# Kernel optimization log

Hardware: AMD Instinct MI355X
Metric: run time of the kernel (lower is better)

Reference implementation:

```python
import jax, jax.numpy as jnp
import numpy as np

EPS = 1e-5
NUM_HEADS = 8

def layer_norm(x, w, b):
    mu = jnp.mean(x, axis=-1, keepdims=True)
    var = jnp.mean(jnp.square(x - mu), axis=-1, keepdims=True)
    return (x - mu) * jax.lax.rsqrt(var + EPS) * w + b

def setup_inputs() -> dict:
    key = jax.random.key(0)
    B, N, C, H, W = 8, 8, 256, 64, 64
    ks = jax.random.split(key, 16)
    p = lambda k, shape: (jax.random.normal(k, shape, dtype=jnp.float32) * 0.02)
    return {
        "mask_tokens": jax.random.normal(ks[0], (B, N, C), dtype=jnp.float32),
        "prompt_embeddings": jax.random.normal(ks[1], (N, B, C, H, W), dtype=jnp.float32),
        "ln_t_w": jnp.ones((C,), jnp.float32), "ln_t_b": jnp.zeros((C,), jnp.float32),
        "ln_p_w": jnp.ones((C,), jnp.float32), "ln_p_b": jnp.zeros((C,), jnp.float32),
        "Wq": p(ks[2], (C, C)), "bq": jnp.zeros((C,), jnp.float32),
        "Wk": p(ks[3], (C, C)), "bk": jnp.zeros((C,), jnp.float32),
        "Wv": p(ks[4], (C, C)), "bv": jnp.zeros((C,), jnp.float32),
        "Wo": p(ks[5], (C, C)), "bo": jnp.zeros((C,), jnp.float32),
        "W1": p(ks[6], (2 * C, C)), "b1": jnp.zeros((2 * C,), jnp.float32),
        "W2": p(ks[7], (C, 2 * C)), "b2": jnp.zeros((C,), jnp.float32),
    }

def reference(mask_tokens, prompt_embeddings, ln_t_w, ln_t_b, ln_p_w, ln_p_b,
              Wq, bq, Wk, bk, Wv, bv, Wo, bo, W1, b1, W2, b2):
    B, N, C = mask_tokens.shape
    Hh = NUM_HEADS
    dh = C // Hh
    scale = 1.0 / jnp.sqrt(jnp.asarray(dh, mask_tokens.dtype))

    normed_tokens = layer_norm(mask_tokens, ln_t_w, ln_t_b)  # [B,N,C]

    # prompt_embeddings: [N,B,C,H,W] -> flatten spatial, move to [B,N,S,C]
    Np, Bp, Cp, H, W = prompt_embeddings.shape
    S = H * W
    prompts = prompt_embeddings.reshape(Np, Bp, Cp, S).transpose(1, 0, 3, 2)  # [B,N,S,C]
    normed_prompts = layer_norm(prompts, ln_p_w, ln_p_b)

    # single-query cross attention per (batch, mask-token), batched over N
    q = (normed_tokens @ Wq.T + bq).reshape(B, N, Hh, dh)          # [B,N,H,dh]
    k = (normed_prompts @ Wk.T + bk).reshape(B, N, S, Hh, dh)       # [B,N,S,H,dh]
    v = (normed_prompts @ Wv.T + bv).reshape(B, N, S, Hh, dh)

    scores = jnp.einsum('bnhd,bnshd->bnhs', q, k) * scale           # [B,N,H,S]
    attn = jax.nn.softmax(scores, axis=-1)
    ctx = jnp.einsum('bnhs,bnshd->bnhd', attn, v).reshape(B, N, C)  # [B,N,C]
    attended = ctx @ Wo.T + bo

    updated = mask_tokens + attended
    hidden = jax.nn.relu(updated @ W1.T + b1)                       # [B,N,2C]
    mlp_out = hidden @ W2.T + b2
    return updated + mlp_out
```

## Files before the change

kernel.cpp:

```cpp
#include <hip/hip_runtime.h>
#include <math.h>

#define C 256
#define S 4096
#define NH 8
#define NSG 64
#define EPS 1e-5f
#define SCALE 0.17677669529663687f

#define TSTR 72
#define PTSTR 72

#define OFF_GWP 0
#define OFF_G   65536
#define OFF_BC  66048
#define OFF_LP  66560
#define OFF_ZP  99328
#define OFF_WEI 132096
#define OFF_MP  263168

typedef __attribute__((ext_vector_type(8))) short short8;
typedef __attribute__((ext_vector_type(4))) float f32x4;
typedef __attribute__((ext_vector_type(4))) float nfloat4;

__device__ __forceinline__ float bf_lo(unsigned int u) {
    return __builtin_bit_cast(float, u << 16);
}
__device__ __forceinline__ float bf_hi(unsigned int u) {
    return __builtin_bit_cast(float, u & 0xffff0000u);
}
__device__ __forceinline__ unsigned int bf_pack(float a, float b) {
    unsigned int ua = (__builtin_bit_cast(unsigned int, a) + 0x8000u) >> 16;
    unsigned int ub = (__builtin_bit_cast(unsigned int, b) + 0x8000u) & 0xffff0000u;
    return ua | ub;
}
__device__ __forceinline__ float bf_round(float a) {
    unsigned int u = (__builtin_bit_cast(unsigned int, a) + 0x8000u) & 0xffff0000u;
    return __builtin_bit_cast(float, u);
}

__global__ __launch_bounds__(256) void k1_prep(
    const float* __restrict__ mt, const float* __restrict__ ln_t_w, const float* __restrict__ ln_t_b,
    const float* __restrict__ ln_p_w, const float* __restrict__ ln_p_b,
    const float* __restrict__ Wq, const float* __restrict__ bq,
    const float* __restrict__ Wk, const float* __restrict__ bk,
    unsigned int* __restrict__ gwp, float* __restrict__ Gv, float* __restrict__ Bc)
{
    int bn  = blockIdx.x;
    int tid = threadIdx.x;
    int wid = tid >> 6, lane = tid & 63;
    __shared__ float nt[C];
    __shared__ float qv[C];
    __shared__ float wks[NH][C];
    __shared__ float red[8];

    float x  = mt[bn * C + tid];
    float s1 = x, s2 = x * x;
    #pragma unroll
    for (int off = 32; off; off >>= 1) {
        s1 += __shfl_xor(s1, off);
        s2 += __shfl_xor(s2, off);
    }
    if (lane == 0) { red[wid] = s1; red[4 + wid] = s2; }
    __syncthreads();
    float mu   = (red[0] + red[1] + red[2] + red[3]) * (1.0f / C);
    float msq  = (red[4] + red[5] + red[6] + red[7]) * (1.0f / C);
    float rstd = rsqrtf(msq - mu * mu + EPS);
    nt[tid] = (x - mu) * rstd * ln_t_w[tid] + ln_t_b[tid];
    __syncthreads();

    {
        float acc = bq[tid];
        const float* wrow = Wq + (size_t)tid * C;
        #pragma unroll 8
        for (int c = 0; c < C; ++c) acc += nt[c] * wrow[c];
        qv[tid] = acc;
    }
    __syncthreads();

    int c = tid;
    #pragma unroll
    for (int h = 0; h < NH; ++h) {
        float a = 0.f;
        #pragma unroll 4
        for (int d = 0; d < 32; ++d) a += qv[h * 32 + d] * Wk[(size_t)(h * 32 + d) * C + c];
        wks[h][c] = a * SCALE;
    }
    __syncthreads();

    for (int i = tid; i < C * 4; i += 256) {
        int cc = i >> 2, pr = i & 3;
        float g0 = ln_p_w[cc] * wks[pr * 2][cc];
        float g1 = ln_p_w[cc] * wks[pr * 2 + 1][cc];
        gwp[(size_t)bn * C * 4 + i] = bf_pack(g0, g1);
    }

    {
        int h = tid >> 5, l32 = tid & 31;
        float g = 0.f, bs = 0.f;
        #pragma unroll
        for (int cc = l32; cc < C; cc += 32) {
            float w = wks[h][cc];
            g  += bf_round(ln_p_w[cc] * w);
            bs += ln_p_b[cc] * w;
        }
        float qb = qv[h * 32 + l32] * bk[h * 32 + l32];
        #pragma unroll
        for (int off = 16; off; off >>= 1) {
            g  += __shfl_xor(g, off);
            bs += __shfl_xor(bs, off);
            qb += __shfl_xor(qb, off);
        }
        if (l32 == 0) {
            Gv[bn * NH + h] = g;
            Bc[bn * NH + h] = bs + qb * SCALE;
        }
    }
}

__global__ __launch_bounds__(256, 3) void kfused(
    const float* __restrict__ pe, const unsigned int* __restrict__ gwp,
    const float* __restrict__ Gv, const float* __restrict__ Bc,
    float* __restrict__ LP, float* __restrict__ ZP, float* __restrict__ Mp)
{
    int blk = blockIdx.x;
    int swz = (blk & 7) * 512 + (blk >> 3);
    int bn  = swz >> 6;
    int sg  = swz & 63;
    int tid = threadIdx.x;
    int w = tid >> 6, lane = tid & 63;
    int cg = lane >> 4, l16 = lane & 15;
    int b = bn >> 3, n = bn & 7;
    const float* xb = pe + ((size_t)(n * 8 + b)) * C * S;
    int s0 = sg * 64;

    __shared__ unsigned short tile[C * TSTR];
    __shared__ unsigned short ptT[16 * PTSTR];
    __shared__ float pbuf[4][64][10];
    __shared__ uint4 gwt[C];

    {
        const uint4* src = reinterpret_cast<const uint4*>(gwp + (size_t)bn * C * 4);
        gwt[tid] = src[tid];
        for (int i = tid; i < 8 * PTSTR; i += 256) ptT[8 * PTSTR + i] = 0;
    }
    __syncthreads();

    {
        const float* xq = xb + (size_t)(w * 64 + cg) * S + s0 + l16 * 4;
        nfloat4 xr[16];
        #pragma unroll
        for (int j = 0; j < 16; ++j)
            xr[j] = __builtin_nontemporal_load(
                        reinterpret_cast<const nfloat4*>(xq + (size_t)(4 * j) * S));

        float sum[4] = {0.f,0.f,0.f,0.f}, sq[4] = {0.f,0.f,0.f,0.f};
        float A[4][NH];
        #pragma unroll
        for (int e = 0; e < 4; ++e)
            #pragma unroll
            for (int h = 0; h < NH; ++h) A[e][h] = 0.f;

        #pragma unroll
        for (int j = 0; j < 16; ++j) {
            int c = w * 64 + 4 * j + cg;
            uint2 pk;
            pk.x = bf_pack(xr[j].x, xr[j].y);
            pk.y = bf_pack(xr[j].z, xr[j].w);
            *reinterpret_cast<uint2*>(&tile[c * TSTR + l16 * 4]) = pk;
            uint4 g = gwt[c];
            float xe[4] = {xr[j].x, xr[j].y, xr[j].z, xr[j].w};
            #pragma unroll
            for (int e = 0; e < 4; ++e) {
                float xx = xe[e];
                sum[e] += xx;
                sq[e]  += xx * xx;
                A[e][0] += bf_lo(g.x) * xx; A[e][1] += bf_hi(g.x) * xx;
                A[e][2] += bf_lo(g.y) * xx; A[e][3] += bf_hi(g.y) * xx;
                A[e][4] += bf_lo(g.z) * xx; A[e][5] += bf_hi(g.z) * xx;
                A[e][6] += bf_lo(g.w) * xx; A[e][7] += bf_hi(g.w) * xx;
            }
        }
        #pragma unroll
        for (int e = 0; e < 4; ++e) {
            sum[e] += __shfl_xor(sum[e], 16); sum[e] += __shfl_xor(sum[e], 32);
            sq[e]  += __shfl_xor(sq[e],  16); sq[e]  += __shfl_xor(sq[e],  32);
            #pragma unroll
            for (int h = 0; h < NH; ++h) {
                A[e][h] += __shfl_xor(A[e][h], 16);
                A[e][h] += __shfl_xor(A[e][h], 32);
            }
        }
        if (cg == 0) {
            #pragma unroll
            for (int e = 0; e < 4; ++e) {
                float* pb = &pbuf[w][l16 * 4 + e][0];
                pb[0] = sum[e];
                pb[1] = sq[e];
                #pragma unroll
                for (int h = 0; h < NH; ++h) pb[2 + h] = A[e][h];
            }
        }
    }
    __syncthreads();

    if (tid < 64) {
        int s = tid;
        float sum = 0.f, sq = 0.f;
        float A[NH];
        #pragma unroll
        for (int h = 0; h < NH; ++h) A[h] = 0.f;
        #pragma unroll
        for (int wv = 0; wv < 4; ++wv) {
            const float* pb = &pbuf[wv][s][0];
            sum += pb[0];
            sq  += pb[1];
            #pragma unroll
            for (int h = 0; h < NH; ++h) A[h] += pb[2 + h];
        }
        float mu   = sum * (1.f / C);
        float var  = sq * (1.f / C) - mu * mu;
        float rs   = rsqrtf(var + EPS);
        float murv = mu * rs;

        float l8[NH], z8[NH];
        #pragma unroll
        for (int h = 0; h < NH; ++h) {
            float p = __expf(rs * A[h] - murv * Gv[bn * NH + h] + Bc[bn * NH + h]);
            ptT[h * PTSTR + s] = (unsigned short)(bf_pack(p * rs, 0.f) & 0xffffu);
            l8[h] = p;
            z8[h] = p * murv;
        }
        #pragma unroll
        for (int h = 0; h < NH; ++h) {
            float l = l8[h], zz = z8[h];
            #pragma unroll
            for (int off = 32; off; off >>= 1) {
                l  += __shfl_xor(l,  off);
                zz += __shfl_xor(zz, off);
            }
            if (tid == 0) {
                LP[(size_t)(bn * NH + h) * NSG + sg] = l;
                ZP[(size_t)(bn * NH + h) * NSG + sg] = zz;
            }
        }
    }
    __syncthreads();

    {
        int mrow = lane & 15;
        int kgrp = lane >> 4;
        float* mp = Mp + (((size_t)sg * 64 + bn) * C) * NH;
        #pragma unroll
        for (int ct = 0; ct < 4; ++ct) {
            int ctile = w * 4 + ct;
            int crow  = ctile * 16 + mrow;
            f32x4 acc = {0.f, 0.f, 0.f, 0.f};
            #pragma unroll
            for (int kc = 0; kc < 2; ++kc) {
                uint4 ap = *reinterpret_cast<const uint4*>(&tile[crow * TSTR + kc * 32 + kgrp * 8]);
                uint4 bp = *reinterpret_cast<const uint4*>(&ptT[mrow * PTSTR + kc * 32 + kgrp * 8]);
                short8 af  = __builtin_bit_cast(short8, ap);
                short8 bfv = __builtin_bit_cast(short8, bp);
                acc = __builtin_amdgcn_mfma_f32_16x16x32_bf16(af, bfv, acc, 0, 0, 0);
            }
            if (mrow < NH) {
                #pragma unroll
                for (int r = 0; r < 4; ++r) {
                    int cl = ctile * 16 + kgrp * 4 + r;
                    mp[cl * NH + mrow] = acc[r];
                }
            }
        }
    }
}

__global__ __launch_bounds__(256) void kfoldM(
    const float* __restrict__ Mp, const float* __restrict__ LP, const float* __restrict__ ZP,
    const float* __restrict__ lpw, const float* __restrict__ lpb, float* __restrict__ weig)
{
    int blk = blockIdx.x;
    int bn = blk >> 3, slice = blk & 7;
    int tid = threadIdx.x;
    __shared__ float ilz[2 * NH];

    if (tid < NH) {
        float L = 0.f, Z = 0.f;
        #pragma unroll 8
        for (int j = 0; j < NSG; ++j) {
            L += LP[(size_t)(bn * NH + tid) * NSG + j];
            Z += ZP[(size_t)(bn * NH + tid) * NSG + j];
        }
        float inv = 1.f / L;
        ilz[tid]      = inv;
        ilz[NH + tid] = Z * inv;
    }
    __syncthreads();

    int c0 = slice * 32;
    const float* base = Mp + ((size_t)bn * C + c0) * NH + tid;
    float acc = 0.f;
    #pragma unroll 8
    for (int sg = 0; sg < NSG; ++sg)
        acc += base[(size_t)sg * 64 * C * NH];

    int c = c0 + (tid >> 3), h = tid & 7;
    weig[(size_t)bn * NH * C + h * C + c] = lpw[c] * (acc * ilz[h] - ilz[NH + h]) + lpb[c];
}

__global__ __launch_bounds__(256) void kpost(
    const float* __restrict__ mt, const float* __restrict__ weig,
    const float* __restrict__ Wv, const float* __restrict__ bv,
    const float* __restrict__ Wo, const float* __restrict__ bo,
    const float* __restrict__ W1, const float* __restrict__ b1,
    const float* __restrict__ W2, const float* __restrict__ b2,
    float* __restrict__ out)
{
    int bn  = blockIdx.x;
    int tid = threadIdx.x;
    __shared__ float wei[NH * C];
    __shared__ float ctxs[C];
    __shared__ float upds[C];
    __shared__ float hid[2 * C];

    for (int v = tid; v < 512; v += 256)
        *reinterpret_cast<float4*>(&wei[v * 4]) =
            *reinterpret_cast<const float4*>(weig + (size_t)bn * NH * C + v * 4);
    __syncthreads();

    {
        int h = tid >> 5;
        float a = bv[tid];
        const float* wrow = Wv + (size_t)tid * C;
        const float* wh   = wei + h * C;
        #pragma unroll 16
        for (int c2 = 0; c2 < C; ++c2) a += wh[c2] * wrow[c2];
        ctxs[tid] = a;
    }
    __syncthreads();

    float att = bo[tid];
    {
        const float* wrow = Wo + (size_t)tid * C;
        #pragma unroll 16
        for (int j = 0; j < C; ++j) att += ctxs[j] * wrow[j];
    }
    float upd = mt[(size_t)bn * C + tid] + att;
    upds[tid] = upd;
    __syncthreads();

    #pragma unroll
    for (int r = 0; r < 2; ++r) {
        int k = tid + r * 256;
        float a = b1[k];
        const float* wrow = W1 + (size_t)k * C;
        #pragma unroll 16
        for (int c2 = 0; c2 < C; ++c2) a += upds[c2] * wrow[c2];
        hid[k] = fmaxf(a, 0.f);
    }
    __syncthreads();

    float a = b2[tid];
    const float* wrow = W2 + (size_t)tid * 2 * C;
    #pragma unroll 16
    for (int k = 0; k < 2 * C; ++k) a += hid[k] * wrow[k];
    out[(size_t)bn * C + tid] = upd + a;
}

extern "C" void kernel_launch(void* const* d_in, const int* in_sizes, int n_in,
                              void* d_out, int out_size, void* d_ws, size_t ws_size,
                              hipStream_t stream)
{
    const float* mt  = (const float*)d_in[0];
    const float* pe  = (const float*)d_in[1];
    const float* ltw = (const float*)d_in[2];
    const float* ltb = (const float*)d_in[3];
    const float* lpw = (const float*)d_in[4];
    const float* lpb = (const float*)d_in[5];
    const float* Wq  = (const float*)d_in[6];
    const float* bq  = (const float*)d_in[7];
    const float* Wk  = (const float*)d_in[8];
    const float* bk  = (const float*)d_in[9];
    const float* Wv  = (const float*)d_in[10];
    const float* bv  = (const float*)d_in[11];
    const float* Wo  = (const float*)d_in[12];
    const float* bo  = (const float*)d_in[13];
    const float* W1  = (const float*)d_in[14];
    const float* b1  = (const float*)d_in[15];
    const float* W2  = (const float*)d_in[16];
    const float* b2  = (const float*)d_in[17];

    float* ws   = (float*)d_ws;
    float* outp = (float*)d_out;

    unsigned int* gwp = (unsigned int*)(ws + OFF_GWP);
    float* Gv         = ws + OFF_G;
    float* Bc         = ws + OFF_BC;
    float* LP         = ws + OFF_LP;
    float* ZP         = ws + OFF_ZP;
    float* weig       = ws + OFF_WEI;
    float* Mp         = ws + OFF_MP;

    k1_prep<<<64,   256, 0, stream>>>(mt, ltw, ltb, lpw, lpb, Wq, bq, Wk, bk, gwp, Gv, Bc);
    kfused <<<4096, 256, 0, stream>>>(pe, gwp, Gv, Bc, LP, ZP, Mp);
    kfoldM <<<512,  256, 0, stream>>>(Mp, LP, ZP, lpw, lpb, weig);
    kpost  <<<64,   256, 0, stream>>>(mt, weig, Wv, bv, Wo, bo, W1, b1, W2, b2, outp);
}
```

Measured before the change: 147.8 us.

## Double spatial tile per block in fused attention kernel, halving grid and partials

Each kfused block now handles 128 spatial positions instead of 64, loading two column strips per thread with 32 float4 loads in flight. Grid shrinks to 2048 blocks, the MFMA K-loop doubles, and the Mp partial count that kfoldM must reduce halves. Softmax partials are still kept per 64-position strip. Launch bounds drop from 3 to 1 block per CU, and the tile LDS grows to about 68 KB. This risks lower occupancy and less latency hiding for the memory-bound stream, in exchange for more work per block and less partial traffic.

```diff
diff --git a/kernel.cpp b/kernel.cpp
--- a/kernel.cpp
+++ b/kernel.cpp
@@ -4,12 +4,13 @@
 #define C 256
 #define S 4096
 #define NH 8
-#define NSG 64
+#define NSGM 32
+#define NSTRIP 64
 #define EPS 1e-5f
 #define SCALE 0.17677669529663687f
 
-#define TSTR 72
-#define PTSTR 72
+#define TSTR 136
+#define PTSTR 136
 
 #define OFF_GWP 0
 #define OFF_G   65536
@@ -118,25 +119,25 @@
     }
 }
 
-__global__ __launch_bounds__(256, 3) void kfused(
+__global__ __launch_bounds__(256, 1) void kfused(
     const float* __restrict__ pe, const unsigned int* __restrict__ gwp,
     const float* __restrict__ Gv, const float* __restrict__ Bc,
     float* __restrict__ LP, float* __restrict__ ZP, float* __restrict__ Mp)
 {
     int blk = blockIdx.x;
-    int swz = (blk & 7) * 512 + (blk >> 3);
-    int bn  = swz >> 6;
-    int sg  = swz & 63;
+    int swz = (blk & 7) * 256 + (blk >> 3);
+    int bn  = swz >> 5;
+    int sg  = swz & 31;
     int tid = threadIdx.x;
     int w = tid >> 6, lane = tid & 63;
     int cg = lane >> 4, l16 = lane & 15;
     int b = bn >> 3, n = bn & 7;
     const float* xb = pe + ((size_t)(n * 8 + b)) * C * S;
-    int s0 = sg * 64;
+    int s0 = sg * 128;
 
     __shared__ unsigned short tile[C * TSTR];
     __shared__ unsigned short ptT[16 * PTSTR];
-    __shared__ float pbuf[4][64][10];
+    __shared__ float pbuf[4][128][11];
     __shared__ uint4 gwt[C];
 
     {
@@ -148,63 +149,95 @@
 
     {
         const float* xq = xb + (size_t)(w * 64 + cg) * S + s0 + l16 * 4;
-        nfloat4 xr[16];
-        #pragma unroll
-        for (int j = 0; j < 16; ++j)
-            xr[j] = __builtin_nontemporal_load(
-                        reinterpret_cast<const nfloat4*>(xq + (size_t)(4 * j) * S));
-
-        float sum[4] = {0.f,0.f,0.f,0.f}, sq[4] = {0.f,0.f,0.f,0.f};
-        float A[4][NH];
+        nfloat4 x0a[8], x1a[8], x0b[8], x1b[8];
+        #pragma unroll
+        for (int q = 0; q < 8; ++q) {
+            const float* p = xq + (size_t)(4 * q) * S;
+            x0a[q] = __builtin_nontemporal_load(reinterpret_cast<const nfloat4*>(p));
+            x1a[q] = __builtin_nontemporal_load(reinterpret_cast<const nfloat4*>(p + 64));
+        }
+        #pragma unroll
+        for (int q = 0; q < 8; ++q) {
+            const float* p = xq + (size_t)(4 * (q + 8)) * S;
+            x0b[q] = __builtin_nontemporal_load(reinterpret_cast<const nfloat4*>(p));
+            x1b[q] = __builtin_nontemporal_load(reinterpret_cast<const nfloat4*>(p + 64));
+        }
+
+        float sum0[4] = {0,0,0,0}, sq0[4] = {0,0,0,0};
+        float sum1[4] = {0,0,0,0}, sq1[4] = {0,0,0,0};
+        float A0[4][NH], A1[4][NH];
         #pragma unroll
         for (int e = 0; e < 4; ++e)
             #pragma unroll
-            for (int h = 0; h < NH; ++h) A[e][h] = 0.f;
-
-        #pragma unroll
-        for (int j = 0; j < 16; ++j) {
-            int c = w * 64 + 4 * j + cg;
-            uint2 pk;
-            pk.x = bf_pack(xr[j].x, xr[j].y);
-            pk.y = bf_pack(xr[j].z, xr[j].w);
-            *reinterpret_cast<uint2*>(&tile[c * TSTR + l16 * 4]) = pk;
-            uint4 g = gwt[c];
-            float xe[4] = {xr[j].x, xr[j].y, xr[j].z, xr[j].w};
+            for (int h = 0; h < NH; ++h) { A0[e][h] = 0.f; A1[e][h] = 0.f; }
+
+        #define PROC(X0, X1, QB)                                                     \
+        {                                                                            \
+            _Pragma("unroll")                                                        \
+            for (int q = 0; q < 8; ++q) {                                            \
+                int cc = w * 64 + 4 * (q + QB) + cg;                                 \
+                uint2 pk0, pk1;                                                      \
+                pk0.x = bf_pack(X0[q].x, X0[q].y);                                   \
+                pk0.y = bf_pack(X0[q].z, X0[q].w);                                   \
+                pk1.x = bf_pack(X1[q].x, X1[q].y);                                   \
+                pk1.y = bf_pack(X1[q].z, X1[q].w);                                   \
+                *reinterpret_cast<uint2*>(&tile[cc * TSTR + l16 * 4]) = pk0;         \
+                *reinterpret_cast<uint2*>(&tile[cc * TSTR + 64 + l16 * 4]) = pk1;    \
+                uint4 g = gwt[cc];                                                   \
+                float ge[8] = {bf_lo(g.x), bf_hi(g.x), bf_lo(g.y), bf_hi(g.y),       \
+                               bf_lo(g.z), bf_hi(g.z), bf_lo(g.w), bf_hi(g.w)};     \
+                float xe0[4] = {X0[q].x, X0[q].y, X0[q].z, X0[q].w};                 \
+                float xe1[4] = {X1[q].x, X1[q].y, X1[q].z, X1[q].w};                 \
+                _Pragma("unroll")                                                    \
+                for (int e = 0; e < 4; ++e) {                                        \
+                    float xx0 = xe0[e], xx1 = xe1[e];                                \
+                    sum0[e] += xx0; sq0[e] += xx0 * xx0;                             \
+                    sum1[e] += xx1; sq1[e] += xx1 * xx1;                             \
+                    _Pragma("unroll")                                                \
+                    for (int h = 0; h < NH; ++h) {                                   \
+                        A0[e][h] += ge[h] * xx0;                                     \
+                        A1[e][h] += ge[h] * xx1;                                     \
+                    }                                                                \
+                }                                                                    \
+            }                                                                        \
+        }
+        PROC(x0a, x1a, 0)
+        PROC(x0b, x1b, 8)
+        #undef PROC
+
+        #pragma unroll
+        for (int e = 0; e < 4; ++e) {
+            sum0[e] += __shfl_xor(sum0[e], 16); sum0[e] += __shfl_xor(sum0[e], 32);
+            sq0[e]  += __shfl_xor(sq0[e],  16); sq0[e]  += __shfl_xor(sq0[e],  32);
+            sum1[e] += __shfl_xor(sum1[e], 16); sum1[e] += __shfl_xor(sum1[e], 32);
+            sq1[e]  += __shfl_xor(sq1[e],  16); sq1[e]  += __shfl_xor(sq1[e],  32);
+            #pragma unroll
+            for (int h = 0; h < NH; ++h) {
+                A0[e][h] += __shfl_xor(A0[e][h], 16);
+                A0[e][h] += __shfl_xor(A0[e][h], 32);
+                A1[e][h] += __shfl_xor(A1[e][h], 16);
+                A1[e][h] += __shfl_xor(A1[e][h], 32);
+            }
+        }
+        if (cg == 0) {
             #pragma unroll
             for (int e = 0; e < 4; ++e) {
-                float xx = xe[e];
-                sum[e] += xx;
-                sq[e]  += xx * xx;
-                A[e][0] += bf_lo(g.x) * xx; A[e][1] += bf_hi(g.x) * xx;
-                A[e][2] += bf_lo(g.y) * xx; A[e][3] += bf_hi(g.y) * xx;
-                A[e][4] += bf_lo(g.z) * xx; A[e][5] += bf_hi(g.z) * xx;
-                A[e][6] += bf_lo(g.w) * xx; A[e][7] += bf_hi(g.w) * xx;
-            }
-        }
-        #pragma unroll
-        for (int e = 0; e < 4; ++e) {
-            sum[e] += __shfl_xor(sum[e], 16); sum[e] += __shfl_xor(sum[e], 32);
-            sq[e]  += __shfl_xor(sq[e],  16); sq[e]  += __shfl_xor(sq[e],  32);
-            #pragma unroll
-            for (int h = 0; h < NH; ++h) {
-                A[e][h] += __shfl_xor(A[e][h], 16);
-                A[e][h] += __shfl_xor(A[e][h], 32);
-            }
-        }
-        if (cg == 0) {
-            #pragma unroll
-            for (int e = 0; e < 4; ++e) {
-                float* pb = &pbuf[w][l16 * 4 + e][0];
-                pb[0] = sum[e];
-                pb[1] = sq[e];
+                float* pb0 = &pbuf[w][l16 * 4 + e][0];
+                pb0[0] = sum0[e];
+                pb0[1] = sq0[e];
                 #pragma unroll
-                for (int h = 0; h < NH; ++h) pb[2 + h] = A[e][h];
-            }
-        }
-    }
-    __syncthreads();
-
-    if (tid < 64) {
+                for (int h = 0; h < NH; ++h) pb0[2 + h] = A0[e][h];
+                float* pb1 = &pbuf[w][64 + l16 * 4 + e][0];
+                pb1[0] = sum1[e];
+                pb1[1] = sq1[e];
+                #pragma unroll
+                for (int h = 0; h < NH; ++h) pb1[2 + h] = A1[e][h];
+            }
+        }
+    }
+    __syncthreads();
+
+    if (tid < 128) {
         int s = tid;
         float sum = 0.f, sq = 0.f;
         float A[NH];
@@ -239,9 +272,10 @@
                 l  += __shfl_xor(l,  off);
                 zz += __shfl_xor(zz, off);
             }
-            if (tid == 0) {
-                LP[(size_t)(bn * NH + h) * NSG + sg] = l;
-                ZP[(size_t)(bn * NH + h) * NSG + sg] = zz;
+            if ((tid & 63) == 0) {
+                int strip = sg * 2 + (tid >> 6);
+                LP[(size_t)(bn * NH + h) * NSTRIP + strip] = l;
+                ZP[(size_t)(bn * NH + h) * NSTRIP + strip] = zz;
             }
         }
     }
@@ -257,7 +291,7 @@
             int crow  = ctile * 16 + mrow;
             f32x4 acc = {0.f, 0.f, 0.f, 0.f};
             #pragma unroll
-            for (int kc = 0; kc < 2; ++kc) {
+            for (int kc = 0; kc < 4; ++kc) {
                 uint4 ap = *reinterpret_cast<const uint4*>(&tile[crow * TSTR + kc * 32 + kgrp * 8]);
                 uint4 bp = *reinterpret_cast<const uint4*>(&ptT[mrow * PTSTR + kc * 32 + kgrp * 8]);
                 short8 af  = __builtin_bit_cast(short8, ap);
@@ -287,9 +321,9 @@
     if (tid < NH) {
         float L = 0.f, Z = 0.f;
         #pragma unroll 8
-        for (int j = 0; j < NSG; ++j) {
-            L += LP[(size_t)(bn * NH + tid) * NSG + j];
-            Z += ZP[(size_t)(bn * NH + tid) * NSG + j];
+        for (int j = 0; j < NSTRIP; ++j) {
+            L += LP[(size_t)(bn * NH + tid) * NSTRIP + j];
+            Z += ZP[(size_t)(bn * NH + tid) * NSTRIP + j];
         }
         float inv = 1.f / L;
         ilz[tid]      = inv;
@@ -301,7 +335,7 @@
     const float* base = Mp + ((size_t)bn * C + c0) * NH + tid;
     float acc = 0.f;
     #pragma unroll 8
-    for (int sg = 0; sg < NSG; ++sg)
+    for (int sg = 0; sg < NSGM; ++sg)
         acc += base[(size_t)sg * 64 * C * NH];
 
     int c = c0 + (tid >> 3), h = tid & 7;
@@ -402,7 +436,7 @@
     float* Mp         = ws + OFF_MP;
 
     k1_prep<<<64,   256, 0, stream>>>(mt, ltw, ltb, lpw, lpb, Wq, bq, Wk, bk, gwp, Gv, Bc);
-    kfused <<<4096, 256, 0, stream>>>(pe, gwp, Gv, Bc, LP, ZP, Mp);
+    kfused <<<2048, 256, 0, stream>>>(pe, gwp, Gv, Bc, LP, ZP, Mp);
     kfoldM <<<512,  256, 0, stream>>>(Mp, LP, ZP, lpw, lpb, weig);
     kpost  <<<64,   256, 0, stream>>>(mt, weig, Wv, bv, Wo, bo, W1, b1, W2, b2, outp);
 }
```

After: 178.8 us. 1.21x slower.
